# Kernel tuning notes

Measured on AMD Instinct MI355X. Metric: run time of the kernel, lower is better.

Reference implementation:

```python
import jax, jax.numpy as jnp
import numpy as np

B, C, H, W = 8, 512, 64, 64
CQ = C // 8  # query/key channels; must equal H==W for the mask broadcast to be valid


def _len_mask(n, length, dtype):
    keep = jnp.arange(n) < length
    return (keep[:, None] & keep[None, :]).astype(dtype)  # [n, n]


def setup_inputs() -> dict:
    key = jax.random.key(0)
    ks = jax.random.split(key, 10)
    s = lambda fan: 1.0 / np.sqrt(fan)
    return {
        "x1": jax.random.normal(ks[0], (B, C, H, W), jnp.float32),
        "x2": jax.random.normal(ks[1], (B, C, H, W), jnp.float32),
        "x3": jax.random.normal(ks[2], (B, C, H, W), jnp.float32),
        "Wq": jax.random.normal(ks[3], (CQ, C), jnp.float32) * s(C),
        "bq": jax.random.normal(ks[4], (CQ,), jnp.float32) * s(C),
        "Wk": jax.random.normal(ks[5], (CQ, C), jnp.float32) * s(C),
        "bk": jax.random.normal(ks[6], (CQ,), jnp.float32) * s(C),
        "Wv": jax.random.normal(ks[7], (C, C), jnp.float32) * s(C),
        "bv": jax.random.normal(ks[8], (C,), jnp.float32) * s(C),
        "gamma": jnp.asarray(0.5, jnp.float32),  # torch init is 0; nonzero to exercise the path
        "length": 32,
    }


def reference(x1, x2, x3, Wq, bq, Wk, bk, Wv, bv, gamma, length):
    b, c, h, w = x1.shape
    dt = x1.dtype
    # 1x1 convs as channel GEMMs
    q = jnp.einsum("bchw,oc->bohw", x1, Wq) + bq[None, :, None, None]  # [B,CQ,H,W]
    k = jnp.einsum("bchw,oc->bohw", x2, Wk) + bk[None, :, None, None]
    v = jnp.einsum("bchw,oc->bohw", x3, Wv) + bv[None, :, None, None]  # [B,C,H,W]

    mH = _len_mask(h, length, dt)  # [H,H] (CQ==H)
    mW = _len_mask(w, length, dt)  # [W,W] (CQ==W)

    # Column (H) attention branch
    qH = jnp.transpose(q, (0, 3, 2, 1)) * mH  # [B,W,H,CQ]
    kH = jnp.transpose(k, (0, 3, 1, 2)) * mH  # [B,W,CQ,H]
    eH = jnp.einsum("bwhc,bwcg->bwhg", qH, kH)  # [B,W,H,H]
    eH = jnp.where(jnp.eye(h, dtype=bool), -jnp.inf, eH)  # diagonal -inf trick
    eH = jnp.transpose(eH, (0, 2, 1, 3))  # [B,H,W,H]

    # Row (W) attention branch
    qW = jnp.transpose(q, (0, 2, 3, 1)) * mW  # [B,H,W,CQ]
    kW = jnp.transpose(k, (0, 2, 1, 3)) * mW  # [B,H,CQ,W]
    eW = jnp.einsum("bhwc,bhcg->bhwg", qW, kW)  # [B,H,W,W]

    att = jax.nn.softmax(jnp.concatenate([eH, eW], axis=3), axis=3)  # [B,H,W,H+W]
    attH = jnp.transpose(att[..., :h], (0, 2, 1, 3))  # [B,W,H,H]
    attW = att[..., h:]  # [B,H,W,W]

    vH = jnp.transpose(v, (0, 3, 1, 2))  # [B,W,C,H]
    vW = jnp.transpose(v, (0, 2, 1, 3))  # [B,H,C,W]
    outH = jnp.einsum("bwcj,bwij->bwci", vH, attH)  # [B,W,C,H]
    outH = jnp.transpose(outH, (0, 2, 3, 1))  # [B,C,H,W]
    outW = jnp.einsum("bhcj,bhij->bhci", vW, attW)  # [B,H,C,W]
    outW = jnp.transpose(outW, (0, 2, 1, 3))  # [B,C,H,W]

    return gamma * (outH + outW) + x1
```

## Files before the change

kernel.cpp:

```cpp
#include <hip/hip_runtime.h>
#include <math.h>
#include <type_traits>

#define CH 512
#define CQ 64
#define HH 64
#define WW 64
#define PP (HH*WW)
#define BB 8

typedef __bf16 bf16x8 __attribute__((ext_vector_type(8)));
typedef __bf16 bf16x4 __attribute__((ext_vector_type(4)));
typedef float  f32x4  __attribute__((ext_vector_type(4)));

__device__ __forceinline__ unsigned lds_off(const void* p) {
  return (unsigned)(size_t)(__attribute__((address_space(3))) const void*)p;
}
__device__ __forceinline__ bf16x4 ds_tr16(unsigned addr) {
  bf16x4 r;
  asm volatile("ds_read_b64_tr_b16 %0, %1" : "=v"(r) : "v"(addr));
  return r;
}

template<int FM, int FN, int NOUT, typename OutT>
__device__ __forceinline__ void proj_body(
    __bf16* AsBase, __bf16* BsBase,
    const float* __restrict__ X, const float* __restrict__ W,
    const float* __restrict__ bias, OutT* __restrict__ Y,
    int mblk, int nblk)
{
  constexpr int BM = 32 * FM;
  constexpr int BN = 32 * FN;
  constexpr int GA = BM / 64;
  constexpr int GB = BN / 64;
  typedef __bf16 (*TileA)[BM][40];
  typedef __bf16 (*TileB)[BN][40];
  TileA As = (TileA)AsBase;
  TileB Bs = (TileB)BsBase;

  const int tid = threadIdx.x;
  const int b     = mblk >> 12;
  const int pbase = mblk & 4095;
  const float* Xb = X + (size_t)b * CH * PP;

  const int l  = tid & 63;
  const int wv = tid >> 6;
  const int wr = wv >> 1, wc = wv & 1;
  const int lm = l & 15, lk = l >> 4;

  int ma[GA], ka[GA];
  #pragma unroll
  for (int gi = 0; gi < GA; ++gi) {
    int g = tid + gi * 256;
    ma[gi] = g % BM;
    ka[gi] = (g / BM) * 8;
  }
  int nb_[GB], kb_[GB];
  #pragma unroll
  for (int gi = 0; gi < GB; ++gi) {
    int g = tid + gi * 256;
    nb_[gi] = g >> 2;
    kb_[gi] = (g & 3) * 8;
  }

  float ra0[GA][8], ra1[GA][8];
  float rb[GB][8];

  auto loadA = [&](float (&ra)[GA][8], int c0) {
    #pragma unroll
    for (int gi = 0; gi < GA; ++gi)
      #pragma unroll
      for (int jj = 0; jj < 8; ++jj)
        ra[gi][jj] = Xb[(size_t)(c0 + ka[gi] + jj) * PP + pbase + ma[gi]];
  };
  auto loadB = [&](int c0) {
    #pragma unroll
    for (int gi = 0; gi < GB; ++gi) {
      const float* src = W + (size_t)(nblk + nb_[gi]) * CH + c0 + kb_[gi];
      float4 f0 = *(const float4*)src;
      float4 f1 = *(const float4*)(src + 4);
      rb[gi][0]=f0.x; rb[gi][1]=f0.y; rb[gi][2]=f0.z; rb[gi][3]=f0.w;
      rb[gi][4]=f1.x; rb[gi][5]=f1.y; rb[gi][6]=f1.z; rb[gi][7]=f1.w;
    }
  };

  f32x4 acc[FM][FN];
  #pragma unroll
  for (int j = 0; j < FN; ++j) {
    float bvj = bias[nblk + wc*FN*16 + j*16 + lm];
    #pragma unroll
    for (int i = 0; i < FM; ++i) {
      acc[i][j][0] = bvj; acc[i][j][1] = bvj;
      acc[i][j][2] = bvj; acc[i][j][3] = bvj;
    }
  }

  auto phase = [&](int t, auto par_c, float (&ra)[GA][8]) {
    constexpr int PAR = decltype(par_c)::value;
    #pragma unroll
    for (int gi = 0; gi < GA; ++gi) {
      bf16x8 hv;
      #pragma unroll
      for (int jj = 0; jj < 8; ++jj) hv[jj] = (__bf16)ra[gi][jj];
      *(bf16x8*)&As[PAR][ma[gi]][ka[gi]] = hv;
    }
    #pragma unroll
    for (int gi = 0; gi < GB; ++gi) {
      bf16x8 hv;
      #pragma unroll
      for (int jj = 0; jj < 8; ++jj) hv[jj] = (__bf16)rb[gi][jj];
      *(bf16x8*)&Bs[PAR][nb_[gi]][kb_[gi]] = hv;
    }
    __syncthreads();
    if (t < 15) loadB((t+1)*32);
    if (t < 14) loadA(ra, (t+2)*32);
    bf16x8 af[FM], bfr[FN];
    #pragma unroll
    for (int i = 0; i < FM; ++i)
      af[i] = *(const bf16x8*)&As[PAR][wr*FM*16 + i*16 + lm][lk*8];
    #pragma unroll
    for (int j = 0; j < FN; ++j)
      bfr[j] = *(const bf16x8*)&Bs[PAR][wc*FN*16 + j*16 + lm][lk*8];
    #pragma unroll
    for (int i = 0; i < FM; ++i)
      #pragma unroll
      for (int j = 0; j < FN; ++j)
        acc[i][j] = __builtin_amdgcn_mfma_f32_16x16x32_bf16(
            af[i], bfr[j], acc[i][j], 0, 0, 0);
  };

  loadA(ra0, 0); loadB(0); loadA(ra1, 32);
  for (int tt = 0; tt < 8; ++tt) {
    phase(2*tt,     std::integral_constant<int,0>{}, ra0);
    phase(2*tt + 1, std::integral_constant<int,1>{}, ra1);
  }

  #pragma unroll
  for (int i = 0; i < FM; ++i) {
    #pragma unroll
    for (int j = 0; j < FN; ++j) {
      #pragma unroll
      for (int r = 0; r < 4; ++r) {
        int mg = mblk + wr*FM*16 + i*16 + lk*4 + r;
        int ng = nblk + wc*FN*16 + j*16 + lm;
        Y[(size_t)mg * NOUT + ng] = (OutT)acc[i][j][r];
      }
    }
  }
}

__global__ __launch_bounds__(256) void proj_all_kernel(
    const float* __restrict__ x3, const float* __restrict__ Wv,
    const float* __restrict__ bv, __bf16* __restrict__ v_t,
    const float* __restrict__ x1, const float* __restrict__ Wq,
    const float* __restrict__ bq, float* __restrict__ q_t,
    const float* __restrict__ x2, const float* __restrict__ Wk,
    const float* __restrict__ bk, float* __restrict__ k_t)
{
  __shared__ __align__(16) __bf16 AsPool[2*128*40];
  __shared__ __align__(16) __bf16 BsPool[2*128*40];
  const int role = blockIdx.x;
  const int mblk = blockIdx.y * 128;
  if (role < 4) {
    proj_body<4,4, CH, __bf16>(AsPool, BsPool, x3, Wv, bv, v_t, mblk, role*128);
  } else if (role == 4) {
    proj_body<4,2, CQ, float >(AsPool, BsPool, x1, Wq, bq, q_t, mblk, 0);
  } else {
    proj_body<4,2, CQ, float >(AsPool, BsPool, x2, Wk, bk, k_t, mblk, 0);
  }
}

__global__ __launch_bounds__(256) void energyH_kernel(
    const float* __restrict__ qt, const float* __restrict__ kt,
    float* __restrict__ eH, const int* __restrict__ len_p)
{
  const int tid = threadIdx.x;
  const int w = blockIdx.x, b = blockIdx.y;
  int L = *len_p; L = L < 0 ? 0 : (L > 64 ? 64 : L);
  __shared__ float Qs[64][68];
  __shared__ float Ks[64][68];
  {
    const int c = tid & 63, hg = tid >> 6;
    const float* qb = qt + ((size_t)b * PP + w) * CQ + c;
    const float* kb = kt + ((size_t)b * PP + w) * CQ + c;
    #pragma unroll
    for (int r = 0; r < 16; ++r) {
      int h = hg*16 + r;
      Qs[h][c] = qb[(size_t)h * WW * CQ];
      Ks[h][c] = kb[(size_t)h * WW * CQ];
    }
  }
  __syncthreads();
  const int g  = tid & 63;
  const int wg = tid >> 6;
  float kreg[64];
  #pragma unroll
  for (int c = 0; c < 64; ++c) kreg[c] = (c < L) ? Ks[g][c] : 0.0f;
  const bool gok = (g < L);
  float* ab = eH + (((size_t)b * HH) * WW + w) * 64 + g;
  for (int r = 0; r < 16; ++r) {
    int h = wg*16 + r;
    float e = 0.0f;
    #pragma unroll
    for (int c4 = 0; c4 < 16; ++c4) {
      float4 q4 = *(const float4*)&Qs[h][4*c4];
      e += q4.x*kreg[4*c4+0] + q4.y*kreg[4*c4+1]
         + q4.z*kreg[4*c4+2] + q4.w*kreg[4*c4+3];
    }
    e = (gok && h < L) ? e : 0.0f;
    if (g == h) e = -INFINITY;
    ab[(size_t)h * WW * 64] = e;
  }
}

__global__ __launch_bounds__(256) void energyW_softmax_kernel(
    const float* __restrict__ qt, const float* __restrict__ kt,
    const float* __restrict__ eH,
    __bf16* __restrict__ attHb, __bf16* __restrict__ attWb,
    const int* __restrict__ len_p)
{
  const int tid = threadIdx.x;
  const int h = blockIdx.x, b = blockIdx.y;
  int L = *len_p; L = L < 0 ? 0 : (L > 64 ? 64 : L);
  __shared__ float Qs[64][68];
  __shared__ float Ks[64][68];
  {
    const int c = tid & 63, wg2 = tid >> 6;
    const float* qb = qt + ((size_t)b * PP + (size_t)h * WW) * CQ + c;
    const float* kb = kt + ((size_t)b * PP + (size_t)h * WW) * CQ + c;
    #pragma unroll
    for (int r = 0; r < 16; ++r) {
      int w = wg2*16 + r;
      Qs[w][c] = qb[(size_t)w * CQ];
      Ks[w][c] = kb[(size_t)w * CQ];
    }
  }
  __syncthreads();
  const int g  = tid & 63;
  const int wg = tid >> 6;
  float kreg[64];
  #pragma unroll
  for (int c = 0; c < 64; ++c) kreg[c] = (c < L) ? Ks[g][c] : 0.0f;
  const bool gok = (g < L);
  const float* ehb = eH + (((size_t)b * HH + h) * WW) * 64 + g;
  __bf16* ahb = attHb + (((size_t)b * HH + h) * WW) * 64 + g;
  __bf16* awb = attWb + (((size_t)b * HH + h) * WW) * 64 + g;
  for (int r = 0; r < 16; ++r) {
    int w = wg*16 + r;
    float e = 0.0f;
    #pragma unroll
    for (int c4 = 0; c4 < 16; ++c4) {
      float4 q4 = *(const float4*)&Qs[w][4*c4];
      e += q4.x*kreg[4*c4+0] + q4.y*kreg[4*c4+1]
         + q4.z*kreg[4*c4+2] + q4.w*kreg[4*c4+3];
    }
    e = (gok && w < L) ? e : 0.0f;
    float eh = ehb[(size_t)w * 64];
    float m = fmaxf(e, eh);
    #pragma unroll
    for (int d = 32; d > 0; d >>= 1) m = fmaxf(m, __shfl_xor(m, d, 64));
    float pe = __expf(e  - m);
    float ph = __expf(eh - m);
    float s = pe + ph;
    #pragma unroll
    for (int d = 32; d > 0; d >>= 1) s += __shfl_xor(s, d, 64);
    float inv = 1.0f / s;
    ahb[(size_t)w * 64] = (__bf16)(ph * inv);
    awb[(size_t)w * 64] = (__bf16)(pe * inv);
  }
}

__device__ __forceinline__ int vsub64_off(int j, int c) {
  int s  = j >> 5;
  int p  = (j >> 2) & 1;
  int t  = ((j & 31) >> 3) * 4 + (j & 3);
  return ((s*2 + p)*4 + (c >> 4))*256 + t*16 + (c & 15);
}

__global__ __launch_bounds__(256) void outH_mfma_kernel(
    const __bf16* __restrict__ attHb, const __bf16* __restrict__ vt,
    __bf16* __restrict__ oH)
{
  const int tid = threadIdx.x;
  const int w = blockIdx.x, cq = blockIdx.y, b = blockIdx.z;
  const int l = tid & 63, wv = tid >> 6;
  const int lm = l & 15, lk = l >> 4;

  __shared__ __align__(16) __bf16 Bs[4096];

  #pragma unroll
  for (int i = 0; i < 2; ++i) {
    int j  = i*32 + (tid >> 3);
    int c0 = (tid & 7) * 8;
    bf16x8 v8 = *(const bf16x8*)(vt + ((size_t)b*PP + (size_t)j*WW + w)*CH + cq*64 + c0);
    *(bf16x8*)&Bs[vsub64_off(j, c0)] = v8;
  }

  const int hrow = wv*16 + lm;
  const __bf16* ab = attHb + (((size_t)b*HH + hrow)*WW + w)*64;
  bf16x8 af[2];
  af[0] = *(const bf16x8*)(ab + lk*8);
  af[1] = *(const bf16x8*)(ab + 32 + lk*8);
  __syncthreads();

  const unsigned bs_base = lds_off(&Bs[0]);
  f32x4 acc[4];
  #pragma unroll
  for (int f = 0; f < 4; ++f) acc[f] = (f32x4){0.f,0.f,0.f,0.f};
  #pragma unroll
  for (int s = 0; s < 2; ++s) {
    bf16x8 bfr[4];
    #pragma unroll
    for (int f = 0; f < 4; ++f) {
      unsigned base = bs_base + (unsigned)((((s*2)*4 + f)*512)) + (unsigned)(l*8);
      bf16x4 t0 = ds_tr16(base);
      bf16x4 t1 = ds_tr16(base + 2048);
      bfr[f] = __builtin_shufflevector(t0, t1, 0,1,2,3,4,5,6,7);
    }
    asm volatile("s_waitcnt lgkmcnt(0)");
    __builtin_amdgcn_sched_barrier(0);
    #pragma unroll
    for (int f = 0; f < 4; ++f)
      acc[f] = __builtin_amdgcn_mfma_f32_16x16x32_bf16(af[s], bfr[f], acc[f], 0,0,0);
  }
  __bf16* ob = oH + (((size_t)b * HH) * WW + w) * CH + cq*64;
  #pragma unroll
  for (int f = 0; f < 4; ++f) {
    #pragma unroll
    for (int r = 0; r < 4; ++r) {
      int h = wv*16 + lk*4 + r;
      ob[(size_t)h * WW * CH + f*16 + lm] = (__bf16)acc[f][r];
    }
  }
}

__global__ __launch_bounds__(256) void outW_final_kernel(
    const __bf16* __restrict__ attWb, const __bf16* __restrict__ vt,
    const __bf16* __restrict__ oH,
    const float* __restrict__ x1, const float* __restrict__ gamma_p,
    float* __restrict__ out)
{
  const int tid = threadIdx.x;
  const int h = blockIdx.x, cq = blockIdx.y, b = blockIdx.z;
  const int l = tid & 63, wv = tid >> 6;
  const int lm = l & 15, lk = l >> 4;
  const float gamma = *gamma_p;

  __shared__ __align__(16) char smem[64*69*4];
  __bf16* Bs = (__bf16*)smem;
  typedef float ScRow[69];
  ScRow* Sc = (ScRow*)smem;

  #pragma unroll
  for (int i = 0; i < 2; ++i) {
    int j  = i*32 + (tid >> 3);
    int c0 = (tid & 7) * 8;
    bf16x8 v8 = *(const bf16x8*)(vt + ((size_t)b*PP + (size_t)h*WW + j)*CH + cq*64 + c0);
    *(bf16x8*)&Bs[vsub64_off(j, c0)] = v8;
  }

  const int wrow = wv*16 + lm;
  const __bf16* ab = attWb + (((size_t)b*HH + h)*WW + wrow)*64;
  bf16x8 af[2];
  af[0] = *(const bf16x8*)(ab + lk*8);
  af[1] = *(const bf16x8*)(ab + 32 + lk*8);

  const int wl = tid & 63, cg = tid >> 6;
  const __bf16* ohb = oH + ((((size_t)b*HH + h) * WW) + wl) * CH + cq*64 + cg*16;
  bf16x8 ohr[2];
  ohr[0] = *(const bf16x8*)(ohb);
  ohr[1] = *(const bf16x8*)(ohb + 8);
  float x1r[16];
  {
    const float* x1b = x1 + ((size_t)b*CH + cq*64 + cg*16)*PP + (size_t)h*WW + wl;
    #pragma unroll
    for (int r2 = 0; r2 < 16; ++r2)
      x1r[r2] = x1b[(size_t)r2 * PP];
  }
  __syncthreads();

  const unsigned bs_base = lds_off(&Bs[0]);
  f32x4 acc[4];
  #pragma unroll
  for (int f = 0; f < 4; ++f) acc[f] = (f32x4){0.f,0.f,0.f,0.f};
  #pragma unroll
  for (int s = 0; s < 2; ++s) {
    bf16x8 bfr[4];
    #pragma unroll
    for (int f = 0; f < 4; ++f) {
      unsigned base = bs_base + (unsigned)((((s*2)*4 + f)*512)) + (unsigned)(l*8);
      bf16x4 t0 = ds_tr16(base);
      bf16x4 t1 = ds_tr16(base + 2048);
      bfr[f] = __builtin_shufflevector(t0, t1, 0,1,2,3,4,5,6,7);
    }
    asm volatile("s_waitcnt lgkmcnt(0)");
    __builtin_amdgcn_sched_barrier(0);
    #pragma unroll
    for (int f = 0; f < 4; ++f)
      acc[f] = __builtin_amdgcn_mfma_f32_16x16x32_bf16(af[s], bfr[f], acc[f], 0,0,0);
  }

  __syncthreads();
  #pragma unroll
  for (int f = 0; f < 4; ++f) {
    #pragma unroll
    for (int r = 0; r < 4; ++r)
      Sc[wv*16 + lk*4 + r][f*16 + lm] = acc[f][r];
  }
  __syncthreads();
  {
    float* obp = out + ((size_t)b*CH + cq*64 + cg*16)*PP + (size_t)h*WW + wl;
    #pragma unroll
    for (int r2 = 0; r2 < 16; ++r2) {
      float oh = (float)ohr[r2 >> 3][r2 & 7];
      obp[(size_t)r2 * PP] = gamma * (Sc[wl][cg*16 + r2] + oh) + x1r[r2];
    }
  }
}

extern "C" void kernel_launch(void* const* d_in, const int* in_sizes, int n_in,
                              void* d_out, int out_size, void* d_ws, size_t ws_size,
                              hipStream_t stream)
{
  const float* x1 = (const float*)d_in[0];
  const float* x2 = (const float*)d_in[1];
  const float* x3 = (const float*)d_in[2];
  const float* Wq = (const float*)d_in[3];
  const float* bq = (const float*)d_in[4];
  const float* Wk = (const float*)d_in[5];
  const float* bk = (const float*)d_in[6];
  const float* Wv = (const float*)d_in[7];
  const float* bv = (const float*)d_in[8];
  const float* gamma = (const float*)d_in[9];
  const int*   len   = (const int*)d_in[10];
  float* out = (float*)d_out;

  float*  q_t   = (float*)d_ws;
  float*  k_t   = q_t + (size_t)BB * PP * CQ;
  float*  eH    = k_t + (size_t)BB * PP * CQ;
  __bf16* attHb = (__bf16*)(eH + (size_t)BB * PP * 64);
  __bf16* attWb = attHb + (size_t)BB * PP * 64;
  __bf16* v_t   = attWb + (size_t)BB * PP * 64;
  __bf16* oH    = v_t + (size_t)BB * PP * CH;

  dim3 blk(256);
  proj_all_kernel<<<dim3(6, BB*PP/128), blk, 0, stream>>>(
      x3, Wv, bv, v_t,  x1, Wq, bq, q_t,  x2, Wk, bk, k_t);

  energyH_kernel<<<dim3(WW, BB), blk, 0, stream>>>(q_t, k_t, eH, len);
  energyW_softmax_kernel<<<dim3(HH, BB), blk, 0, stream>>>(q_t, k_t, eH, attHb, attWb, len);
  outH_mfma_kernel<<<dim3(WW, 8, BB), blk, 0, stream>>>(attHb, v_t, oH);
  outW_final_kernel<<<dim3(HH, 8, BB), blk, 0, stream>>>(attWb, v_t, oH, x1, gamma, out);
}
```

Measured before the change: 158.5 us.

## Use 512-thread projection blocks and store q/k projections as bf16

Launches the projection GEMM with 512 threads (8 waves in a 2x4 layout) over the same 128-row tiles. Each thread now loads one A group and a smaller B slice, which cuts per-thread registers and raises the number of waves per block. The q and k projection outputs are stored as bf16 instead of fp32, halving their workspace traffic in the two energy kernels. This lowers the precision of q/k going into the attention energies.

```diff
diff --git a/kernel.cpp b/kernel.cpp
--- a/kernel.cpp
+++ b/kernel.cpp
@@ -22,17 +22,16 @@
   return r;
 }
 
-template<int FM, int FN, int NOUT, typename OutT>
+template<int FN, int NOUT, typename OutT>
 __device__ __forceinline__ void proj_body(
     __bf16* AsBase, __bf16* BsBase,
     const float* __restrict__ X, const float* __restrict__ W,
     const float* __restrict__ bias, OutT* __restrict__ Y,
     int mblk, int nblk)
 {
-  constexpr int BM = 32 * FM;
-  constexpr int BN = 32 * FN;
-  constexpr int GA = BM / 64;
-  constexpr int GB = BN / 64;
+  constexpr int BM = 128;
+  constexpr int BN = FN * 64;
+  constexpr int BE = (BN * 32) / 512;
   typedef __bf16 (*TileA)[BM][40];
   typedef __bf16 (*TileB)[BN][40];
   TileA As = (TileA)AsBase;
@@ -45,84 +44,74 @@
 
   const int l  = tid & 63;
   const int wv = tid >> 6;
-  const int wr = wv >> 1, wc = wv & 1;
+  const int wr = wv >> 2, wc = wv & 3;
   const int lm = l & 15, lk = l >> 4;
 
-  int ma[GA], ka[GA];
-  #pragma unroll
-  for (int gi = 0; gi < GA; ++gi) {
-    int g = tid + gi * 256;
-    ma[gi] = g % BM;
-    ka[gi] = (g / BM) * 8;
-  }
-  int nb_[GB], kb_[GB];
-  #pragma unroll
-  for (int gi = 0; gi < GB; ++gi) {
-    int g = tid + gi * 256;
-    nb_[gi] = g >> 2;
-    kb_[gi] = (g & 3) * 8;
-  }
-
-  float ra0[GA][8], ra1[GA][8];
-  float rb[GB][8];
-
-  auto loadA = [&](float (&ra)[GA][8], int c0) {
-    #pragma unroll
-    for (int gi = 0; gi < GA; ++gi)
-      #pragma unroll
-      for (int jj = 0; jj < 8; ++jj)
-        ra[gi][jj] = Xb[(size_t)(c0 + ka[gi] + jj) * PP + pbase + ma[gi]];
+  const int ma = tid & 127;
+  const int ka = (tid >> 7) * 8;
+  const int nb = (BE == 8) ? (tid & 127) : (tid & 63);
+  const int kb = (BE == 8) ? ((tid >> 7) * 8) : ((tid >> 6) * 4);
+
+  float ra0[8], ra1[8];
+  float rb[BE];
+
+  auto loadA = [&](float (&ra)[8], int c0) {
+    #pragma unroll
+    for (int jj = 0; jj < 8; ++jj)
+      ra[jj] = Xb[(size_t)(c0 + ka + jj) * PP + pbase + ma];
   };
   auto loadB = [&](int c0) {
-    #pragma unroll
-    for (int gi = 0; gi < GB; ++gi) {
-      const float* src = W + (size_t)(nblk + nb_[gi]) * CH + c0 + kb_[gi];
-      float4 f0 = *(const float4*)src;
+    const float* src = W + (size_t)(nblk + nb) * CH + c0 + kb;
+    float4 f0 = *(const float4*)src;
+    rb[0]=f0.x; rb[1]=f0.y; rb[2]=f0.z; rb[3]=f0.w;
+    if constexpr (BE == 8) {
       float4 f1 = *(const float4*)(src + 4);
-      rb[gi][0]=f0.x; rb[gi][1]=f0.y; rb[gi][2]=f0.z; rb[gi][3]=f0.w;
-      rb[gi][4]=f1.x; rb[gi][5]=f1.y; rb[gi][6]=f1.z; rb[gi][7]=f1.w;
+      rb[4]=f1.x; rb[5]=f1.y; rb[6]=f1.z; rb[7]=f1.w;
     }
   };
 
-  f32x4 acc[FM][FN];
+  f32x4 acc[4][FN];
   #pragma unroll
   for (int j = 0; j < FN; ++j) {
     float bvj = bias[nblk + wc*FN*16 + j*16 + lm];
     #pragma unroll
-    for (int i = 0; i < FM; ++i) {
+    for (int i = 0; i < 4; ++i) {
       acc[i][j][0] = bvj; acc[i][j][1] = bvj;
       acc[i][j][2] = bvj; acc[i][j][3] = bvj;
     }
   }
 
-  auto phase = [&](int t, auto par_c, float (&ra)[GA][8]) {
+  auto phase = [&](int t, auto par_c, float (&ra)[8]) {
     constexpr int PAR = decltype(par_c)::value;
-    #pragma unroll
-    for (int gi = 0; gi < GA; ++gi) {
+    {
       bf16x8 hv;
       #pragma unroll
-      for (int jj = 0; jj < 8; ++jj) hv[jj] = (__bf16)ra[gi][jj];
-      *(bf16x8*)&As[PAR][ma[gi]][ka[gi]] = hv;
-    }
-    #pragma unroll
-    for (int gi = 0; gi < GB; ++gi) {
+      for (int jj = 0; jj < 8; ++jj) hv[jj] = (__bf16)ra[jj];
+      *(bf16x8*)&As[PAR][ma][ka] = hv;
+    }
+    if constexpr (BE == 8) {
       bf16x8 hv;
       #pragma unroll
-      for (int jj = 0; jj < 8; ++jj) hv[jj] = (__bf16)rb[gi][jj];
-      *(bf16x8*)&Bs[PAR][nb_[gi]][kb_[gi]] = hv;
+      for (int jj = 0; jj < 8; ++jj) hv[jj] = (__bf16)rb[jj];
+      *(bf16x8*)&Bs[PAR][nb][kb] = hv;
+    } else {
+      bf16x4 hv;
+      #pragma unroll
+      for (int jj = 0; jj < 4; ++jj) hv[jj] = (__bf16)rb[jj];
+      *(bf16x4*)&Bs[PAR][nb][kb] = hv;
     }
     __syncthreads();
     if (t < 15) loadB((t+1)*32);
     if (t < 14) loadA(ra, (t+2)*32);
-    bf16x8 af[FM], bfr[FN];
-    #pragma unroll
-    for (int i = 0; i < FM; ++i)
-      af[i] = *(const bf16x8*)&As[PAR][wr*FM*16 + i*16 + lm][lk*8];
+    bf16x8 af[4], bfr[FN];
+    #pragma unroll
+    for (int i = 0; i < 4; ++i)
+      af[i] = *(const bf16x8*)&As[PAR][wr*64 + i*16 + lm][lk*8];
     #pragma unroll
     for (int j = 0; j < FN; ++j)
       bfr[j] = *(const bf16x8*)&Bs[PAR][wc*FN*16 + j*16 + lm][lk*8];
     #pragma unroll
-    for (int i = 0; i < FM; ++i)
+    for (int i = 0; i < 4; ++i)
       #pragma unroll
       for (int j = 0; j < FN; ++j)
         acc[i][j] = __builtin_amdgcn_mfma_f32_16x16x32_bf16(
@@ -136,12 +125,12 @@
   }
 
   #pragma unroll
-  for (int i = 0; i < FM; ++i) {
+  for (int i = 0; i < 4; ++i) {
     #pragma unroll
     for (int j = 0; j < FN; ++j) {
       #pragma unroll
       for (int r = 0; r < 4; ++r) {
-        int mg = mblk + wr*FM*16 + i*16 + lk*4 + r;
+        int mg = mblk + wr*64 + i*16 + lk*4 + r;
         int ng = nblk + wc*FN*16 + j*16 + lm;
         Y[(size_t)mg * NOUT + ng] = (OutT)acc[i][j][r];
       }
@@ -149,29 +138,29 @@
   }
 }
 
-__global__ __launch_bounds__(256) void proj_all_kernel(
+__global__ __launch_bounds__(512) void proj_all_kernel(
     const float* __restrict__ x3, const float* __restrict__ Wv,
     const float* __restrict__ bv, __bf16* __restrict__ v_t,
     const float* __restrict__ x1, const float* __restrict__ Wq,
-    const float* __restrict__ bq, float* __restrict__ q_t,
+    const float* __restrict__ bq, __bf16* __restrict__ q_t,
     const float* __restrict__ x2, const float* __restrict__ Wk,
-    const float* __restrict__ bk, float* __restrict__ k_t)
+    const float* __restrict__ bk, __bf16* __restrict__ k_t)
 {
   __shared__ __align__(16) __bf16 AsPool[2*128*40];
   __shared__ __align__(16) __bf16 BsPool[2*128*40];
   const int role = blockIdx.x;
   const int mblk = blockIdx.y * 128;
   if (role < 4) {
-    proj_body<4,4, CH, __bf16>(AsPool, BsPool, x3, Wv, bv, v_t, mblk, role*128);
+    proj_body<2, CH, __bf16>(AsPool, BsPool, x3, Wv, bv, v_t, mblk, role*128);
   } else if (role == 4) {
-    proj_body<4,2, CQ, float >(AsPool, BsPool, x1, Wq, bq, q_t, mblk, 0);
+    proj_body<1, CQ, __bf16>(AsPool, BsPool, x1, Wq, bq, q_t, mblk, 0);
   } else {
-    proj_body<4,2, CQ, float >(AsPool, BsPool, x2, Wk, bk, k_t, mblk, 0);
+    proj_body<1, CQ, __bf16>(AsPool, BsPool, x2, Wk, bk, k_t, mblk, 0);
   }
 }
 
 __global__ __launch_bounds__(256) void energyH_kernel(
-    const float* __restrict__ qt, const float* __restrict__ kt,
+    const __bf16* __restrict__ qt, const __bf16* __restrict__ kt,
     float* __restrict__ eH, const int* __restrict__ len_p)
 {
   const int tid = threadIdx.x;
@@ -181,13 +170,13 @@
   __shared__ float Ks[64][68];
   {
     const int c = tid & 63, hg = tid >> 6;
-    const float* qb = qt + ((size_t)b * PP + w) * CQ + c;
-    const float* kb = kt + ((size_t)b * PP + w) * CQ + c;
+    const __bf16* qb = qt + ((size_t)b * PP + w) * CQ + c;
+    const __bf16* kb = kt + ((size_t)b * PP + w) * CQ + c;
     #pragma unroll
     for (int r = 0; r < 16; ++r) {
       int h = hg*16 + r;
-      Qs[h][c] = qb[(size_t)h * WW * CQ];
-      Ks[h][c] = kb[(size_t)h * WW * CQ];
+      Qs[h][c] = (float)qb[(size_t)h * WW * CQ];
+      Ks[h][c] = (float)kb[(size_t)h * WW * CQ];
     }
   }
   __syncthreads();
@@ -214,7 +203,7 @@
 }
 
 __global__ __launch_bounds__(256) void energyW_softmax_kernel(
-    const float* __restrict__ qt, const float* __restrict__ kt,
+    const __bf16* __restrict__ qt, const __bf16* __restrict__ kt,
     const float* __restrict__ eH,
     __bf16* __restrict__ attHb, __bf16* __restrict__ attWb,
     const int* __restrict__ len_p)
@@ -226,13 +215,13 @@
   __shared__ float Ks[64][68];
   {
     const int c = tid & 63, wg2 = tid >> 6;
-    const float* qb = qt + ((size_t)b * PP + (size_t)h * WW) * CQ + c;
-    const float* kb = kt + ((size_t)b * PP + (size_t)h * WW) * CQ + c;
+    const __bf16* qb = qt + ((size_t)b * PP + (size_t)h * WW) * CQ + c;
+    const __bf16* kb = kt + ((size_t)b * PP + (size_t)h * WW) * CQ + c;
     #pragma unroll
     for (int r = 0; r < 16; ++r) {
       int w = wg2*16 + r;
-      Qs[w][c] = qb[(size_t)w * CQ];
-      Ks[w][c] = kb[(size_t)w * CQ];
+      Qs[w][c] = (float)qb[(size_t)w * CQ];
+      Ks[w][c] = (float)kb[(size_t)w * CQ];
     }
   }
   __syncthreads();
@@ -435,18 +424,18 @@
   const int*   len   = (const int*)d_in[10];
   float* out = (float*)d_out;
 
-  float*  q_t   = (float*)d_ws;
-  float*  k_t   = q_t + (size_t)BB * PP * CQ;
-  float*  eH    = k_t + (size_t)BB * PP * CQ;
+  __bf16* q_t   = (__bf16*)d_ws;
+  __bf16* k_t   = q_t + (size_t)BB * PP * CQ;
+  float*  eH    = (float*)(k_t + (size_t)BB * PP * CQ);
   __bf16* attHb = (__bf16*)(eH + (size_t)BB * PP * 64);
   __bf16* attWb = attHb + (size_t)BB * PP * 64;
   __bf16* v_t   = attWb + (size_t)BB * PP * 64;
   __bf16* oH    = v_t + (size_t)BB * PP * CH;
 
+  proj_all_kernel<<<dim3(6, BB*PP/128), dim3(512), 0, stream>>>(
+      x3, Wv, bv, v_t,  x1, Wq, bq, q_t,  x2, Wk, bk, k_t);
+
   dim3 blk(256);
-  proj_all_kernel<<<dim3(6, BB*PP/128), blk, 0, stream>>>(
-      x3, Wv, bv, v_t,  x1, Wq, bq, q_t,  x2, Wk, bk, k_t);
-
   energyH_kernel<<<dim3(WW, BB), blk, 0, stream>>>(q_t, k_t, eH, len);
   energyW_softmax_kernel<<<dim3(HH, BB), blk, 0, stream>>>(q_t, k_t, eH, attHb, attWb, len);
   outH_mfma_kernel<<<dim3(WW, 8, BB), blk, 0, stream>>>(attHb, v_t, oH);
```

New measurement: 169.8 us. +7.1%, slower.
